# Kernel tuning notes

Measured on AMD Instinct MI355X. Metric: run time of the kernel, lower is better.

## Reference

```python
import jax, jax.numpy as jnp
import numpy as np

N = 4096
D_MODEL = 512


def setup_inputs() -> dict:
    key = jax.random.key(0)
    ks = jax.random.split(key, 5)
    scale = 1.0 / np.sqrt(D_MODEL)
    return {
        "x": jax.random.normal(ks[0], (N, D_MODEL), dtype=jnp.float32),
        "Wq": jax.random.normal(ks[1], (D_MODEL, D_MODEL), dtype=jnp.float32) * scale,
        "Wk": jax.random.normal(ks[2], (D_MODEL, D_MODEL), dtype=jnp.float32) * scale,
        "Wv": jax.random.normal(ks[3], (D_MODEL, D_MODEL), dtype=jnp.float32) * scale,
        "Ws": jax.random.normal(ks[4], (1, D_MODEL), dtype=jnp.float32) * scale,
    }


def reference(x, Wq, Wk, Wv, Ws):
    # x: [N, d]; torch nn.Linear(bias=False) computes x @ W.T
    Q = x @ Wq.T  # [N, d]
    K = x @ Wk.T  # [N, d]
    V = x @ Wv.T  # [N, d]
    sigma = jnp.clip(x @ Ws.T, 0.001, 1.0)  # [N, 1]

    # prior association: Gaussian kernel over |i - j| with per-row sigma
    pos = jnp.arange(sigma.shape[0], dtype=jnp.float32)
    diff = jnp.abs(pos[:, None] - pos[None, :])  # [N, N]
    gaussian = jnp.exp(-0.5 * (diff / sigma) ** 2) / jnp.sqrt(2.0 * jnp.pi * sigma)
    P = gaussian / (gaussian.sum(axis=1, keepdims=True) + 1e-8)

    scale = jnp.sqrt(jnp.float32(x.shape[-1]))
    S = jax.nn.softmax((Q @ K.T) / scale, axis=-1)  # [N, N]
    Z = S @ V  # [N, d]
    return Z, P, S
```

## Files before the change

### kernel.cpp

```cpp
#include <hip/hip_runtime.h>
#include <math.h>

#define N_TOK 4096
#define DM 512

typedef _Float16 f16x8 __attribute__((ext_vector_type(8)));
typedef _Float16 f16x4 __attribute__((ext_vector_type(4)));
typedef float f32x4 __attribute__((ext_vector_type(4)));

__device__ __forceinline__ void async_ld16(const ushort* g, ushort* l) {
  __builtin_amdgcn_global_load_lds(
      (const __attribute__((address_space(1))) void*)g,
      (__attribute__((address_space(3))) void*)l, 16, 0, 0);
}

__global__ __launch_bounds__(256) void pack_sigma(
    const float* __restrict__ x, const float* __restrict__ Wq,
    const float* __restrict__ Wk, const float* __restrict__ Wv,
    const float* __restrict__ Ws, _Float16* __restrict__ x16,
    _Float16* __restrict__ Wc16, float* __restrict__ sg,
    float* __restrict__ denom) {
  const int b = blockIdx.x;
  const int t = threadIdx.x;
  if (b < 2048) {
    int i = b * 1024 + t * 4;
    float4 v = *(const float4*)&x[i];
    f16x4 o;
    o.x = (_Float16)v.x; o.y = (_Float16)v.y;
    o.z = (_Float16)v.z; o.w = (_Float16)v.w;
    *(f16x4*)&x16[i] = o;
    int col = (t * 4) & 511;
    float4 w = *(const float4*)&Ws[col];
    float p = v.x * w.x + v.y * w.y + v.z * w.z + v.w * w.w;
    __shared__ float red[256];
    red[t] = p;
    __syncthreads();
    int lt = t & 127;
    for (int off = 64; off > 0; off >>= 1) {
      if (lt < off) red[t] += red[t + off];
      __syncthreads();
    }
    if (lt == 0) {
      float s = red[t];
      sg[2 * b + (t >> 7)] = fminf(fmaxf(s, 0.001f), 1.0f);
    }
  } else if (b < 2816) {
    int e = (b - 2048) * 1024 + t * 4;
    const float* src;
    int le = e & (DM * DM - 1);
    if (e < DM * DM) src = Wq + le;
    else if (e < 2 * DM * DM) src = Wk + le;
    else src = Wv + le;
    float4 v = *(const float4*)src;
    f16x4 o;
    o.x = (_Float16)v.x; o.y = (_Float16)v.y;
    o.z = (_Float16)v.z; o.w = (_Float16)v.w;
    *(f16x4*)&Wc16[e] = o;
  } else {
    float4 zz = {0.f, 0.f, 0.f, 0.f};
#pragma unroll
    for (int k = 0; k < 4; ++k) *(float4*)&denom[(t * 4 + k * 1024)] = zz;
  }
}

template <int EPI>
__global__ __launch_bounds__(256) void mfma_f16(
    const _Float16* __restrict__ A, int lda, const _Float16* __restrict__ B,
    int ldb, int K, float scale, float* __restrict__ Cf, int ldc,
    _Float16* __restrict__ D0, _Float16* __restrict__ D1,
    _Float16* __restrict__ D2, _Float16* __restrict__ Part16,
    float* __restrict__ denom) {
  __shared__ _Float16 lds[2 * 128 * 32];
  __shared__ float dinv[128];
  _Float16* Ah = lds;
  _Float16* Bh = lds + 128 * 32;

  const int t = threadIdx.x;
  const int w = t >> 6, L = t & 63;
  const int wm = (w >> 1) * 64, wn = (w & 1) * 64;
  const int row = L & 15, quad = L >> 4;
  const int bm = blockIdx.y * 128, bn = blockIdx.x * 128;
  const int kbase = blockIdx.z * K;

  if (EPI == 2 && t < 128) dinv[t] = 1.0f / denom[bm + t];

  f32x4 acc[4][4] = {{}};

  const int c0 = t, c1 = t + 256;
  const int r0 = c0 >> 2, o0 = (c0 & 3) * 8;
  const int r1 = r0 + 64;

  const ushort* ga0 = (const ushort*)(A + (size_t)(bm + r0) * lda + kbase + o0);
  const ushort* ga1 = (const ushort*)(A + (size_t)(bm + r1) * lda + kbase + o0);
  const ushort* gb0 = (const ushort*)(B + (size_t)(bn + r0) * ldb + kbase + o0);
  const ushort* gb1 = (const ushort*)(B + (size_t)(bn + r1) * ldb + kbase + o0);

  for (int k0 = 0; k0 < K; k0 += 32) {
    async_ld16(ga0, (ushort*)(Ah + c0 * 8));
    async_ld16(ga1, (ushort*)(Ah + c1 * 8));
    async_ld16(gb0, (ushort*)(Bh + c0 * 8));
    async_ld16(gb1, (ushort*)(Bh + c1 * 8));
    ga0 += 32; ga1 += 32; gb0 += 32; gb1 += 32;
    __syncthreads();

    f16x8 a0[4], b0[4];
#pragma unroll
    for (int i = 0; i < 4; ++i)
      a0[i] = *(const f16x8*)&Ah[(wm + i * 16 + row) * 32 + quad * 8];
#pragma unroll
    for (int j = 0; j < 4; ++j)
      b0[j] = *(const f16x8*)&Bh[(wn + j * 16 + row) * 32 + quad * 8];
#pragma unroll
    for (int i = 0; i < 4; ++i)
#pragma unroll
      for (int j = 0; j < 4; ++j)
        acc[i][j] = __builtin_amdgcn_mfma_f32_16x16x32_f16(a0[i], b0[j],
                                                           acc[i][j], 0, 0, 0);
    __syncthreads();
  }

  if (EPI == 1) {
    const int region = bn >> 9;
    _Float16* D = (region == 0) ? D0 : ((region == 1) ? D1 : D2);
#pragma unroll
    for (int i = 0; i < 4; ++i)
#pragma unroll
      for (int j = 0; j < 4; ++j)
#pragma unroll
        for (int r = 0; r < 4; ++r) {
          int gr = bm + wm + i * 16 + quad * 4 + r;
          int nn = (bn & 511) + wn + j * 16 + row;
          D[(size_t)gr * 512 + nn] = (_Float16)acc[i][j][r];
        }
  } else if (EPI == 4) {
#pragma unroll
    for (int i = 0; i < 4; ++i)
#pragma unroll
      for (int r = 0; r < 4; ++r) {
        int gr = bm + wm + i * 16 + quad * 4 + r;
        float s = 0.f;
#pragma unroll
        for (int j = 0; j < 4; ++j) {
          float e = __expf(acc[i][j][r] * scale);
          int gc = bn + wn + j * 16 + row;
          D0[(size_t)gr * ldc + gc] = (_Float16)e;
          s += e;
        }
        s += __shfl_xor(s, 1);
        s += __shfl_xor(s, 2);
        s += __shfl_xor(s, 4);
        s += __shfl_xor(s, 8);
        if (row == 0) atomicAdd(&denom[gr], s);
      }
  } else {
    const int z = blockIdx.z;
#pragma unroll
    for (int i = 0; i < 4; ++i)
#pragma unroll
      for (int j = 0; j < 4; ++j)
#pragma unroll
        for (int r = 0; r < 4; ++r) {
          int lr = wm + i * 16 + quad * 4 + r;
          int gr = bm + lr;
          int gc = bn + wn + j * 16 + row;
          float v = acc[i][j][r] * dinv[lr];
          if (z == 0)
            Cf[(size_t)gr * ldc + gc] = v;
          else
            Part16[(size_t)(z - 1) * 2097152 + (size_t)gr * ldc + gc] =
                (_Float16)v;
        }
  }
}

__global__ __launch_bounds__(256) void transpose16(
    const _Float16* __restrict__ V16, _Float16* __restrict__ VT) {
  __shared__ _Float16 T[32][34];
  const int t = threadIdx.x;
  const int r = t >> 3, c4 = (t & 7) * 4;
  f16x4 v = *(const f16x4*)&V16[(size_t)(blockIdx.y * 32 + r) * 512 +
                                blockIdx.x * 32 + c4];
  T[r][c4] = v.x; T[r][c4 + 1] = v.y; T[r][c4 + 2] = v.z; T[r][c4 + 3] = v.w;
  __syncthreads();
  f16x4 o;
  o.x = T[c4][r]; o.y = T[c4 + 1][r]; o.z = T[c4 + 2][r]; o.w = T[c4 + 3][r];
  *(f16x4*)&VT[(size_t)(blockIdx.x * 32 + r) * 4096 + blockIdx.y * 32 + c4] = o;
}

__global__ __launch_bounds__(256) void tail_kernel(
    const float* __restrict__ sigma, float* __restrict__ P,
    float* __restrict__ Z, const _Float16* __restrict__ Part16,
    const _Float16* __restrict__ E16, const float* __restrict__ denom,
    float* __restrict__ S) {
  const int t = threadIdx.x;
  const int b = blockIdx.x;
  if (b >= 6144) {
    int idx = (b - 6144) * 1024 + t * 4;
    int rw = (b - 6144) >> 2;
    float inv = 1.0f / denom[rw];
    f16x4 e = *(const f16x4*)&E16[idx];
    float4 o;
    o.x = (float)e.x * inv; o.y = (float)e.y * inv;
    o.z = (float)e.z * inv; o.w = (float)e.w * inv;
    *(float4*)&S[idx] = o;
    return;
  }
  if (b >= 4096) {
    int i = (b - 4096) * 1024 + t * 4;
    float4 z = *(const float4*)&Z[i];
    f16x4 a = *(const f16x4*)&Part16[i];
    f16x4 c = *(const f16x4*)&Part16[2097152 + i];
    f16x4 d = *(const f16x4*)&Part16[2 * 2097152 + i];
    z.x += (float)a.x + (float)c.x + (float)d.x;
    z.y += (float)a.y + (float)c.y + (float)d.y;
    z.z += (float)a.z + (float)c.z + (float)d.z;
    z.w += (float)a.w + (float)c.w + (float)d.w;
    *(float4*)&Z[i] = z;
    return;
  }
  __shared__ float red[256];
  const int i = b;
  const float sg = sigma[i];
  const float inv2 = -0.5f / (sg * sg);
  const float c = rsqrtf(6.283185307179586f * sg);
  float4 g[4];
  float sum = 0.f;
#pragma unroll
  for (int r = 0; r < 4; ++r) {
    int j = r * 1024 + t * 4;
    float d0 = (float)(i - j);
    float d1 = (float)(i - j - 1);
    float d2 = (float)(i - j - 2);
    float d3 = (float)(i - j - 3);
    g[r].x = __expf(inv2 * d0 * d0) * c;
    g[r].y = __expf(inv2 * d1 * d1) * c;
    g[r].z = __expf(inv2 * d2 * d2) * c;
    g[r].w = __expf(inv2 * d3 * d3) * c;
    sum += g[r].x + g[r].y + g[r].z + g[r].w;
  }
  red[t] = sum;
  __syncthreads();
  for (int off = 128; off > 0; off >>= 1) {
    if (t < off) red[t] += red[t + off];
    __syncthreads();
  }
  const float inv = 1.0f / (red[0] + 1e-8f);
  float* Prow = P + (size_t)i * N_TOK;
#pragma unroll
  for (int r = 0; r < 4; ++r) {
    g[r].x *= inv; g[r].y *= inv; g[r].z *= inv; g[r].w *= inv;
    *(float4*)&Prow[r * 1024 + t * 4] = g[r];
  }
}

extern "C" void kernel_launch(void* const* d_in, const int* in_sizes, int n_in,
                              void* d_out, int out_size, void* d_ws,
                              size_t ws_size, hipStream_t stream) {
  const float* x = (const float*)d_in[0];
  const float* Wq = (const float*)d_in[1];
  const float* Wk = (const float*)d_in[2];
  const float* Wv = (const float*)d_in[3];
  const float* Ws = (const float*)d_in[4];

  float* out = (float*)d_out;
  float* Z = out;
  float* Pout = Z + (size_t)N_TOK * DM;
  float* S = Pout + (size_t)N_TOK * N_TOK;

  const size_t E = (size_t)N_TOK * DM;
  _Float16* Q16 = (_Float16*)Pout;
  _Float16* K16 = Q16 + E;
  _Float16* V16 = K16 + E;
  _Float16* VT16 = V16 + E;

  _Float16* x16 = (_Float16*)d_ws;
  _Float16* Wc16 = x16 + E;
  float* sg = (float*)(Wc16 + 3 * DM * DM);
  float* denom = sg + 4096;
  _Float16* Part16 = (_Float16*)(denom + 4096);
  _Float16* E16 = Part16 + 3 * E;

  const dim3 blk(256);

  pack_sigma<<<2817, blk, 0, stream>>>(x, Wq, Wk, Wv, Ws, x16, Wc16, sg, denom);

  mfma_f16<1><<<dim3(12, 32), blk, 0, stream>>>(
      x16, DM, Wc16, DM, DM, 1.0f, nullptr, 0, Q16, K16, V16, nullptr, nullptr);

  transpose16<<<dim3(16, 128), blk, 0, stream>>>(V16, VT16);

  mfma_f16<4><<<dim3(32, 32), blk, 0, stream>>>(
      Q16, DM, K16, DM, DM, 1.0f / sqrtf((float)DM), nullptr, N_TOK, E16,
      nullptr, nullptr, nullptr, denom);

  mfma_f16<2><<<dim3(4, 32, 4), blk, 0, stream>>>(
      E16, N_TOK, VT16, N_TOK, N_TOK / 4, 1.0f, Z, DM, nullptr, nullptr,
      nullptr, Part16, denom);

  tail_kernel<<<4096 + 2048 + 16384, blk, 0, stream>>>(sg, Pout, Z, Part16,
                                                       E16, denom, S);
}
```

Measured before the change: 264.7 us.

## Fuse S normalization into SV GEMM and skip negligible Gaussian terms

Writes the normalized softmax matrix S directly from the LDS-staged E tiles inside the S@V GEMM, using only the blockIdx.x==0 column blocks, and drops the separate S-normalization blocks from the tail kernel. This removes a full extra read of the fp16 E matrix. The Gaussian prior now evaluates exp only within a distance of 16 of the diagonal, since sigma is at most 1 and terms further out underflow. In exchange, a subset of GEMM blocks does extra store work, which may unbalance that kernel.

```diff
diff --git a/kernel.cpp b/kernel.cpp
--- a/kernel.cpp
+++ b/kernel.cpp
@@ -69,7 +69,7 @@
     int ldb, int K, float scale, float* __restrict__ Cf, int ldc,
     _Float16* __restrict__ D0, _Float16* __restrict__ D1,
     _Float16* __restrict__ D2, _Float16* __restrict__ Part16,
-    float* __restrict__ denom) {
+    float* __restrict__ denom, float* __restrict__ Sout) {
   __shared__ _Float16 lds[2 * 128 * 32];
   __shared__ float dinv[128];
   _Float16* Ah = lds;
@@ -116,6 +116,28 @@
       for (int j = 0; j < 4; ++j)
         acc[i][j] = __builtin_amdgcn_mfma_f32_16x16x32_f16(a0[i], b0[j],
                                                            acc[i][j], 0, 0, 0);
+    if (EPI == 2) {
+      if (blockIdx.x == 0) {
+        const int lr = t >> 1, co = (t & 1) * 16;
+        f16x8 e0 = *(const f16x8*)&Ah[lr * 32 + co];
+        f16x8 e1 = *(const f16x8*)&Ah[lr * 32 + co + 8];
+        const float di = dinv[lr];
+        float* Sp = Sout + (size_t)(bm + lr) * N_TOK + kbase + k0 + co;
+        float4 o0, o1, o2, o3;
+        o0.x = (float)e0[0] * di; o0.y = (float)e0[1] * di;
+        o0.z = (float)e0[2] * di; o0.w = (float)e0[3] * di;
+        o1.x = (float)e0[4] * di; o1.y = (float)e0[5] * di;
+        o1.z = (float)e0[6] * di; o1.w = (float)e0[7] * di;
+        o2.x = (float)e1[0] * di; o2.y = (float)e1[1] * di;
+        o2.z = (float)e1[2] * di; o2.w = (float)e1[3] * di;
+        o3.x = (float)e1[4] * di; o3.y = (float)e1[5] * di;
+        o3.z = (float)e1[6] * di; o3.w = (float)e1[7] * di;
+        *(float4*)&Sp[0] = o0;
+        *(float4*)&Sp[4] = o1;
+        *(float4*)&Sp[8] = o2;
+        *(float4*)&Sp[12] = o3;
+      }
+    }
     __syncthreads();
   }
 
@@ -189,22 +211,9 @@
 
 __global__ __launch_bounds__(256) void tail_kernel(
     const float* __restrict__ sigma, float* __restrict__ P,
-    float* __restrict__ Z, const _Float16* __restrict__ Part16,
-    const _Float16* __restrict__ E16, const float* __restrict__ denom,
-    float* __restrict__ S) {
+    float* __restrict__ Z, const _Float16* __restrict__ Part16) {
   const int t = threadIdx.x;
   const int b = blockIdx.x;
-  if (b >= 6144) {
-    int idx = (b - 6144) * 1024 + t * 4;
-    int rw = (b - 6144) >> 2;
-    float inv = 1.0f / denom[rw];
-    f16x4 e = *(const f16x4*)&E16[idx];
-    float4 o;
-    o.x = (float)e.x * inv; o.y = (float)e.y * inv;
-    o.z = (float)e.z * inv; o.w = (float)e.w * inv;
-    *(float4*)&S[idx] = o;
-    return;
-  }
   if (b >= 4096) {
     int i = (b - 4096) * 1024 + t * 4;
     float4 z = *(const float4*)&Z[i];
@@ -228,14 +237,20 @@
 #pragma unroll
   for (int r = 0; r < 4; ++r) {
     int j = r * 1024 + t * 4;
-    float d0 = (float)(i - j);
-    float d1 = (float)(i - j - 1);
-    float d2 = (float)(i - j - 2);
-    float d3 = (float)(i - j - 3);
-    g[r].x = __expf(inv2 * d0 * d0) * c;
-    g[r].y = __expf(inv2 * d1 * d1) * c;
-    g[r].z = __expf(inv2 * d2 * d2) * c;
-    g[r].w = __expf(inv2 * d3 * d3) * c;
+    g[r].x = 0.f; g[r].y = 0.f; g[r].z = 0.f; g[r].w = 0.f;
+    if (j + 3 >= i - 16 && j <= i + 16) {
+#pragma unroll
+      for (int kk = 0; kk < 4; ++kk) {
+        int d = i - (j + kk);
+        if (d * d <= 256) {
+          float e = __expf(inv2 * (float)(d * d)) * c;
+          if (kk == 0) g[r].x = e;
+          else if (kk == 1) g[r].y = e;
+          else if (kk == 2) g[r].z = e;
+          else g[r].w = e;
+        }
+      }
+    }
     sum += g[r].x + g[r].y + g[r].z + g[r].w;
   }
   red[t] = sum;
@@ -285,18 +300,18 @@
   pack_sigma<<<2817, blk, 0, stream>>>(x, Wq, Wk, Wv, Ws, x16, Wc16, sg, denom);
 
   mfma_f16<1><<<dim3(12, 32), blk, 0, stream>>>(
-      x16, DM, Wc16, DM, DM, 1.0f, nullptr, 0, Q16, K16, V16, nullptr, nullptr);
+      x16, DM, Wc16, DM, DM, 1.0f, nullptr, 0, Q16, K16, V16, nullptr,
+      nullptr, nullptr);
 
   transpose16<<<dim3(16, 128), blk, 0, stream>>>(V16, VT16);
 
   mfma_f16<4><<<dim3(32, 32), blk, 0, stream>>>(
       Q16, DM, K16, DM, DM, 1.0f / sqrtf((float)DM), nullptr, N_TOK, E16,
-      nullptr, nullptr, nullptr, denom);
+      nullptr, nullptr, nullptr, denom, nullptr);
 
   mfma_f16<2><<<dim3(4, 32, 4), blk, 0, stream>>>(
       E16, N_TOK, VT16, N_TOK, N_TOK / 4, 1.0f, Z, DM, nullptr, nullptr,
-      nullptr, Part16, denom);
-
-  tail_kernel<<<4096 + 2048 + 16384, blk, 0, stream>>>(sg, Pout, Z, Part16,
-                                                       E16, denom, S);
-}
+      nullptr, Part16, denom, S);
+
+  tail_kernel<<<4096 + 2048, blk, 0, stream>>>(sg, Pout, Z, Part16);
+}
```

New measurement: 313.4 us. +18.4%, slower.
